# Kernel tuning notes

Hardware: AMD Instinct MI355X
Metric: run time of the kernel (lower is better)

Reference implementation:

```python
import jax, jax.numpy as jnp
import numpy as np

N = 8192          # number of particles
CUTOFF = 0.5      # self.cutoff (final filter uses d_ij <= cutoff)


def setup_inputs() -> dict:
    key = jax.random.key(0)
    k1, _ = jax.random.split(key)
    positions = jax.random.normal(k1, (N, 3), dtype=jnp.float32)
    box_vectors = jnp.eye(3, dtype=jnp.float32)  # orthogonal box, lengths 1.0
    iu, ju = np.triu_indices(N, k=1)             # all unique pairs i < j (as in _init_pairs)
    i_pairs = jnp.asarray(iu, dtype=jnp.int32)
    j_pairs = jnp.asarray(ju, dtype=jnp.int32)
    return {"positions": positions, "box_vectors": box_vectors,
            "i_pairs": i_pairs, "j_pairs": j_pairs, "is_periodic": 1}


def reference(positions, box_vectors, i_pairs, j_pairs, is_periodic):
    # OrthogonalDisplacementFunction: r_ij = x_i - x_j, wrapped into the box
    r_ij = positions[i_pairs] - positions[j_pairs]          # [P, 3]
    if is_periodic:
        box_lengths = jnp.diagonal(box_vectors)             # [3] (orthogonal box)
        half = box_lengths * 0.5
        r_ij = jnp.remainder(r_ij + half, box_lengths) - half
    d_ij = jnp.linalg.norm(r_ij, axis=1, keepdims=True)     # [P, 1]
    # Cutoff filter. torch compacts with boolean indexing (data-dependent shape);
    # for a jit-compatible fixed-shape reference we return a validity mask and
    # zero the entries of filtered-out pairs (only_unique_pairs=True branch).
    mask = d_ij[:, 0] <= CUTOFF                              # [P]
    pair_indices = jnp.stack([i_pairs, j_pairs])             # [2, P]
    r_out = jnp.where(mask[:, None], r_ij, 0.0)
    d_out = jnp.where(mask[:, None], d_ij, 0.0)
    return pair_indices, d_out, r_out, mask
```

## Files before the change

### kernel.cpp

```cpp
#include <hip/hip_runtime.h>
#include <math.h>


__device__ __forceinline__ float bf2f(unsigned short h) {
    return __uint_as_float(((unsigned)h) << 16);
}

__device__ __forceinline__ float rem_np(float x, float L) {
    float fm = fmodf(x, L);
    if (fm != 0.0f && ((fm < 0.0f) != (L < 0.0f))) fm += L;
    return fm;
}

__device__ __forceinline__ float rem1_np(float x) {
    float fm = __fsub_rn(x, truncf(x));
    if (fm < 0.0f) fm = __fadd_rn(fm, 1.0f);
    return fm;
}

template <bool F32>
__device__ __forceinline__ void load_pos(const void* __restrict__ pos, int idx,
                                         float& x, float& y, float& z) {
    if (F32) {
        const float* q = (const float*)pos + 3 * idx;
        x = q[0]; y = q[1]; z = q[2];
    } else {
        const unsigned short* q = (const unsigned short*)pos + 3 * idx;
        x = bf2f(q[0]); y = bf2f(q[1]); z = bf2f(q[2]);
    }
}

template <bool F32>
__device__ __forceinline__ void body(const void* __restrict__ pos,
                                     float Lx, float Ly, float Lz,
                                     bool periodic, bool unit, int N, long long P,
                                     int i, int j, long long t,
                                     float* __restrict__ out) {
    const float hx = __fmul_rn(Lx, 0.5f);
    const float hy = __fmul_rn(Ly, 0.5f);
    const float hz = __fmul_rn(Lz, 0.5f);

    float fi[4], fj[4], fd[4], fm[4], fr[12];

    float xi, yi, zi;
    load_pos<F32>(pos, i, xi, yi, zi);

#pragma unroll
    for (int k = 0; k < 4; ++k) {
        float xj, yj, zj;
        load_pos<F32>(pos, j, xj, yj, zj);
        float rx = __fsub_rn(xi, xj);
        float ry = __fsub_rn(yi, yj);
        float rz = __fsub_rn(zi, zj);
        if (periodic) {
            float vx = __fadd_rn(rx, hx);
            float vy = __fadd_rn(ry, hy);
            float vz = __fadd_rn(rz, hz);
            if (unit) {
                rx = __fsub_rn(rem1_np(vx), hx);
                ry = __fsub_rn(rem1_np(vy), hy);
                rz = __fsub_rn(rem1_np(vz), hz);
            } else {
                rx = __fsub_rn(rem_np(vx, Lx), hx);
                ry = __fsub_rn(rem_np(vy, Ly), hy);
                rz = __fsub_rn(rem_np(vz, Lz), hz);
            }
        }
        float d2 = __fadd_rn(__fadd_rn(__fmul_rn(rx, rx), __fmul_rn(ry, ry)),
                             __fmul_rn(rz, rz));
        float d = sqrtf(d2);
        bool m = (d <= 0.5f);

        fi[k] = (float)i;
        fj[k] = (float)j;
        fd[k] = m ? d : 0.0f;
        fm[k] = m ? 1.0f : 0.0f;
        fr[3 * k + 0] = m ? rx : 0.0f;
        fr[3 * k + 1] = m ? ry : 0.0f;
        fr[3 * k + 2] = m ? rz : 0.0f;

        if (k < 3) {
            ++j;
            if (j >= N) {
                ++i;
                j = i + 1;
                load_pos<F32>(pos, i, xi, yi, zi);
            }
        }
    }

    ((float4*)(out))[t]          = make_float4(fi[0], fi[1], fi[2], fi[3]);
    ((float4*)(out + P))[t]      = make_float4(fj[0], fj[1], fj[2], fj[3]);
    ((float4*)(out + 2 * P))[t]  = make_float4(fd[0], fd[1], fd[2], fd[3]);
    float4* orr = (float4*)(out + 3 * P);
    orr[3 * t + 0] = make_float4(fr[0], fr[1], fr[2], fr[3]);
    orr[3 * t + 1] = make_float4(fr[4], fr[5], fr[6], fr[7]);
    orr[3 * t + 2] = make_float4(fr[8], fr[9], fr[10], fr[11]);
    ((float4*)(out + 6 * P))[t]  = make_float4(fm[0], fm[1], fm[2], fm[3]);
}

__global__ __launch_bounds__(256) void nsq_kernel(const void* __restrict__ pos,
                                                  const unsigned* __restrict__ box_raw,
                                                  const int* __restrict__ isper,
                                                  float* __restrict__ out,
                                                  int N, long long P) {
    long long t = (long long)blockIdx.x * blockDim.x + threadIdx.x;
    long long p0 = t << 2;
    if (p0 >= P) return;

    const bool f32 = (box_raw[0] == 0x3F800000u);

    float Lx, Ly, Lz;
    if (f32) {
        const float* b = (const float*)box_raw;
        Lx = b[0]; Ly = b[4]; Lz = b[8];
    } else {
        const unsigned short* b = (const unsigned short*)box_raw;
        Lx = bf2f(b[0]); Ly = bf2f(b[4]); Lz = bf2f(b[8]);
    }
    const bool periodic = (isper[0] != 0);
    const bool unit = (Lx == 1.0f) && (Ly == 1.0f) && (Lz == 1.0f);

    const double M = 2.0 * (double)N - 1.0;
    int i = (int)((M - sqrt(M * M - 8.0 * (double)p0)) * 0.5);
    if (i < 0) i = 0;
    if (i > N - 2) i = N - 2;
    auto off = [N](long long a) { return a * (2LL * N - 1 - a) / 2; };
    while (i < N - 2 && off(i + 1) <= p0) ++i;
    while (i > 0 && off(i) > p0) --i;
    int j = (int)((long long)i + 1 + (p0 - off(i)));

    if (f32)
        body<true>(pos, Lx, Ly, Lz, periodic, unit, N, P, i, j, t, out);
    else
        body<false>(pos, Lx, Ly, Lz, periodic, unit, N, P, i, j, t, out);
}

extern "C" void kernel_launch(void* const* d_in, const int* in_sizes, int n_in,
                              void* d_out, int out_size, void* d_ws, size_t ws_size,
                              hipStream_t stream) {
    const void* pos = d_in[0];
    const unsigned* box = (const unsigned*)d_in[1];
    const int* isper = (const int*)d_in[4];

    long long P = (long long)out_size / 7;
    int N = in_sizes[0] / 3;

    long long nthreads = (P + 3) >> 2;
    int blocks = (int)((nthreads + 255) / 256);
    nsq_kernel<<<blocks, 256, 0, stream>>>(pos, box, isper, (float*)d_out, N, P);
}
```

Baseline: 1.029 ms.

## Stage bf16 positions in LDS with persistent tiles and coalesced r stores

Adds a persistent-grid kernel for the bf16 case that copies all particle positions into shared memory once per block, then loops over tiles of pairs reading positions from LDS. The displacement output is transposed through a shared buffer so r_ij is written with fully coalesced float4 stores. A grid-stride fallback kernel handles f32 or unsupported shapes, and both kernels are always launched, each exiting early when it is not the one responsible. The cost is an extra kernel launch, a large shared-memory footprint that limits occupancy, and two block barriers per tile.

Result: no change. 1.041 ms (+1.1%).

```diff
diff --git a/kernel.cpp b/kernel.cpp
--- a/kernel.cpp
+++ b/kernel.cpp
@@ -2,8 +2,19 @@
 #include <math.h>
 
 
+#define TPB 256
+#define PPT 4
+#define TILE (TPB * PPT)
+#define NMAX 8192
+
 __device__ __forceinline__ float bf2f(unsigned short h) {
     return __uint_as_float(((unsigned)h) << 16);
+}
+
+__device__ __forceinline__ float rem1_np(float x) {
+    float fm = __fsub_rn(x, truncf(x));
+    if (fm < 0.0f) fm = __fadd_rn(fm, 1.0f);
+    return fm;
 }
 
 __device__ __forceinline__ float rem_np(float x, float L) {
@@ -12,103 +23,186 @@
     return fm;
 }
 
-__device__ __forceinline__ float rem1_np(float x) {
-    float fm = __fsub_rn(x, truncf(x));
-    if (fm < 0.0f) fm = __fadd_rn(fm, 1.0f);
-    return fm;
-}
-
-template <bool F32>
-__device__ __forceinline__ void load_pos(const void* __restrict__ pos, int idx,
-                                         float& x, float& y, float& z) {
-    if (F32) {
-        const float* q = (const float*)pos + 3 * idx;
-        x = q[0]; y = q[1]; z = q[2];
-    } else {
-        const unsigned short* q = (const unsigned short*)pos + 3 * idx;
-        x = bf2f(q[0]); y = bf2f(q[1]); z = bf2f(q[2]);
-    }
-}
-
-template <bool F32>
-__device__ __forceinline__ void body(const void* __restrict__ pos,
-                                     float Lx, float Ly, float Lz,
-                                     bool periodic, bool unit, int N, long long P,
-                                     int i, int j, long long t,
-                                     float* __restrict__ out) {
-    const float hx = __fmul_rn(Lx, 0.5f);
-    const float hy = __fmul_rn(Ly, 0.5f);
-    const float hz = __fmul_rn(Lz, 0.5f);
-
-    float fi[4], fj[4], fd[4], fm[4], fr[12];
-
-    float xi, yi, zi;
-    load_pos<F32>(pos, i, xi, yi, zi);
-
-#pragma unroll
-    for (int k = 0; k < 4; ++k) {
-        float xj, yj, zj;
-        load_pos<F32>(pos, j, xj, yj, zj);
-        float rx = __fsub_rn(xi, xj);
-        float ry = __fsub_rn(yi, yj);
-        float rz = __fsub_rn(zi, zj);
-        if (periodic) {
-            float vx = __fadd_rn(rx, hx);
-            float vy = __fadd_rn(ry, hy);
-            float vz = __fadd_rn(rz, hz);
-            if (unit) {
-                rx = __fsub_rn(rem1_np(vx), hx);
-                ry = __fsub_rn(rem1_np(vy), hy);
-                rz = __fsub_rn(rem1_np(vz), hz);
+__device__ __forceinline__ void inv_tri(long long p0, int N, int& i, int& j) {
+    const double M = 2.0 * (double)N - 1.0;
+    int ii = (int)((M - sqrt(M * M - 8.0 * (double)p0)) * 0.5);
+    if (ii < 0) ii = 0;
+    if (ii > N - 2) ii = N - 2;
+    auto off = [N](long long a) { return a * (2LL * N - 1 - a) / 2; };
+    while (ii < N - 2 && off(ii + 1) <= p0) ++ii;
+    while (ii > 0 && off(ii) > p0) --ii;
+    i = ii;
+    j = (int)((long long)ii + 1 + (p0 - off(ii)));
+}
+
+__device__ __forceinline__ void pair_math(float xi, float yi, float zi,
+                                          float xj, float yj, float zj,
+                                          float hx, float hy, float hz,
+                                          float Lx, float Ly, float Lz,
+                                          bool periodic, bool unit,
+                                          float& rx, float& ry, float& rz,
+                                          float& d, bool& m) {
+    rx = __fsub_rn(xi, xj);
+    ry = __fsub_rn(yi, yj);
+    rz = __fsub_rn(zi, zj);
+    if (periodic) {
+        float vx = __fadd_rn(rx, hx), vy = __fadd_rn(ry, hy), vz = __fadd_rn(rz, hz);
+        if (unit) {
+            rx = __fsub_rn(rem1_np(vx), hx);
+            ry = __fsub_rn(rem1_np(vy), hy);
+            rz = __fsub_rn(rem1_np(vz), hz);
+        } else {
+            rx = __fsub_rn(rem_np(vx, Lx), hx);
+            ry = __fsub_rn(rem_np(vy, Ly), hy);
+            rz = __fsub_rn(rem_np(vz, Lz), hz);
+        }
+    }
+    float d2 = __fadd_rn(__fadd_rn(__fmul_rn(rx, rx), __fmul_rn(ry, ry)),
+                         __fmul_rn(rz, rz));
+    d = sqrtf(d2);
+    m = (d <= 0.5f);
+}
+
+__global__ __launch_bounds__(TPB) void nsq_bf16_lds(
+        const unsigned short* __restrict__ pos,
+        const unsigned* __restrict__ box_raw,
+        const int* __restrict__ isper,
+        float* __restrict__ out,
+        int N, long long P, int n_tiles) {
+    if (box_raw[0] == 0x3F800000u) return;
+
+    __shared__ unsigned short s_pos[3 * NMAX];
+    __shared__ float s_r[TPB * 13];
+
+    {
+        const uint4* src = (const uint4*)pos;
+        uint4* dst = (uint4*)s_pos;
+        int n16 = (3 * N) / 8;
+        for (int idx = threadIdx.x; idx < n16; idx += TPB) dst[idx] = src[idx];
+    }
+
+    const unsigned short* b = (const unsigned short*)box_raw;
+    const float Lx = bf2f(b[0]), Ly = bf2f(b[4]), Lz = bf2f(b[8]);
+    const float hx = __fmul_rn(Lx, 0.5f), hy = __fmul_rn(Ly, 0.5f), hz = __fmul_rn(Lz, 0.5f);
+    const bool periodic = (isper[0] != 0);
+    const bool unit = (Lx == 1.0f) && (Ly == 1.0f) && (Lz == 1.0f);
+
+    __syncthreads();
+
+    float* out_i = out;
+    float* out_j = out + P;
+    float* out_d = out + 2 * P;
+    float* out_r = out + 3 * P;
+    float* out_m = out + 6 * P;
+
+    for (int tile = blockIdx.x; tile < n_tiles; tile += gridDim.x) {
+        const long long tp0 = (long long)tile * TILE;
+        const long long p0 = tp0 + (long long)threadIdx.x * PPT;
+        const int vpairs = (int)((P - tp0 < (long long)TILE) ? (P - tp0) : (long long)TILE);
+
+        float fi[PPT], fj[PPT], fd[PPT], fm[PPT], fr[3 * PPT];
+
+        int i = 0, j = 1;
+        if (p0 < P) inv_tri(p0, N, i, j);
+
+        float xi = bf2f(s_pos[3 * i + 0]);
+        float yi = bf2f(s_pos[3 * i + 1]);
+        float zi = bf2f(s_pos[3 * i + 2]);
+
+#pragma unroll
+        for (int k = 0; k < PPT; ++k) {
+            const bool valid = (p0 + k) < P;
+            int jj = j < N ? j : (N - 1);
+            float xj = bf2f(s_pos[3 * jj + 0]);
+            float yj = bf2f(s_pos[3 * jj + 1]);
+            float zj = bf2f(s_pos[3 * jj + 2]);
+            float rx, ry, rz, d; bool m;
+            pair_math(xi, yi, zi, xj, yj, zj, hx, hy, hz, Lx, Ly, Lz,
+                      periodic, unit, rx, ry, rz, d, m);
+            m = m && valid;
+            fi[k] = valid ? (float)i : 0.0f;
+            fj[k] = valid ? (float)jj : 0.0f;
+            fd[k] = m ? d : 0.0f;
+            fm[k] = m ? 1.0f : 0.0f;
+            fr[3 * k + 0] = m ? rx : 0.0f;
+            fr[3 * k + 1] = m ? ry : 0.0f;
+            fr[3 * k + 2] = m ? rz : 0.0f;
+            if (k < PPT - 1) {
+                ++j;
+                if (j >= N) {
+                    if (i < N - 2) {
+                        ++i;
+                        j = i + 1;
+                        xi = bf2f(s_pos[3 * i + 0]);
+                        yi = bf2f(s_pos[3 * i + 1]);
+                        zi = bf2f(s_pos[3 * i + 2]);
+                    } else {
+                        j = N - 1;
+                    }
+                }
+            }
+        }
+
+        const long long t4 = p0 >> 2;
+        if (p0 + PPT <= P) {
+            ((float4*)out_i)[t4] = make_float4(fi[0], fi[1], fi[2], fi[3]);
+            ((float4*)out_j)[t4] = make_float4(fj[0], fj[1], fj[2], fj[3]);
+            ((float4*)out_d)[t4] = make_float4(fd[0], fd[1], fd[2], fd[3]);
+            ((float4*)out_m)[t4] = make_float4(fm[0], fm[1], fm[2], fm[3]);
+        } else if (p0 < P) {
+            for (int k = 0; k < PPT; ++k) {
+                if (p0 + k < P) {
+                    out_i[p0 + k] = fi[k];
+                    out_j[p0 + k] = fj[k];
+                    out_d[p0 + k] = fd[k];
+                    out_m[p0 + k] = fm[k];
+                }
+            }
+        }
+
+        __syncthreads();
+#pragma unroll
+        for (int k = 0; k < PPT; ++k) {
+            s_r[13 * threadIdx.x + 3 * k + 0] = fr[3 * k + 0];
+            s_r[13 * threadIdx.x + 3 * k + 1] = fr[3 * k + 1];
+            s_r[13 * threadIdx.x + 3 * k + 2] = fr[3 * k + 2];
+        }
+        __syncthreads();
+
+        const long long R0 = 3 * tp0;
+        const int vfloats = 3 * vpairs;
+#pragma unroll
+        for (int s = 0; s < 3; ++s) {
+            const int u0 = 4 * (s * TPB + threadIdx.x);
+            if (u0 + 3 < vfloats || (vpairs == TILE)) {
+                float v[4];
+#pragma unroll
+                for (int e = 0; e < 4; ++e) {
+                    int u = u0 + e, q = u / 3, c = u - 3 * q;
+                    v[e] = s_r[13 * (q >> 2) + 3 * (q & 3) + c];
+                }
+                ((float4*)(out_r + R0))[u0 >> 2] = make_float4(v[0], v[1], v[2], v[3]);
             } else {
-                rx = __fsub_rn(rem_np(vx, Lx), hx);
-                ry = __fsub_rn(rem_np(vy, Ly), hy);
-                rz = __fsub_rn(rem_np(vz, Lz), hz);
-            }
-        }
-        float d2 = __fadd_rn(__fadd_rn(__fmul_rn(rx, rx), __fmul_rn(ry, ry)),
-                             __fmul_rn(rz, rz));
-        float d = sqrtf(d2);
-        bool m = (d <= 0.5f);
-
-        fi[k] = (float)i;
-        fj[k] = (float)j;
-        fd[k] = m ? d : 0.0f;
-        fm[k] = m ? 1.0f : 0.0f;
-        fr[3 * k + 0] = m ? rx : 0.0f;
-        fr[3 * k + 1] = m ? ry : 0.0f;
-        fr[3 * k + 2] = m ? rz : 0.0f;
-
-        if (k < 3) {
-            ++j;
-            if (j >= N) {
-                ++i;
-                j = i + 1;
-                load_pos<F32>(pos, i, xi, yi, zi);
-            }
-        }
-    }
-
-    ((float4*)(out))[t]          = make_float4(fi[0], fi[1], fi[2], fi[3]);
-    ((float4*)(out + P))[t]      = make_float4(fj[0], fj[1], fj[2], fj[3]);
-    ((float4*)(out + 2 * P))[t]  = make_float4(fd[0], fd[1], fd[2], fd[3]);
-    float4* orr = (float4*)(out + 3 * P);
-    orr[3 * t + 0] = make_float4(fr[0], fr[1], fr[2], fr[3]);
-    orr[3 * t + 1] = make_float4(fr[4], fr[5], fr[6], fr[7]);
-    orr[3 * t + 2] = make_float4(fr[8], fr[9], fr[10], fr[11]);
-    ((float4*)(out + 6 * P))[t]  = make_float4(fm[0], fm[1], fm[2], fm[3]);
-}
-
-__global__ __launch_bounds__(256) void nsq_kernel(const void* __restrict__ pos,
-                                                  const unsigned* __restrict__ box_raw,
-                                                  const int* __restrict__ isper,
-                                                  float* __restrict__ out,
-                                                  int N, long long P) {
-    long long t = (long long)blockIdx.x * blockDim.x + threadIdx.x;
-    long long p0 = t << 2;
-    if (p0 >= P) return;
-
+                for (int e = 0; e < 4; ++e) {
+                    int u = u0 + e;
+                    if (u < vfloats) {
+                        int q = u / 3, c = u - 3 * q;
+                        out_r[R0 + u] = s_r[13 * (q >> 2) + 3 * (q & 3) + c];
+                    }
+                }
+            }
+        }
+    }
+}
+
+__global__ __launch_bounds__(TPB) void nsq_fallback(
+        const void* __restrict__ pos,
+        const unsigned* __restrict__ box_raw,
+        const int* __restrict__ isper,
+        float* __restrict__ out,
+        int N, long long P, int fast_handled) {
     const bool f32 = (box_raw[0] == 0x3F800000u);
+    if (fast_handled && !f32) return;
 
     float Lx, Ly, Lz;
     if (f32) {
@@ -118,22 +212,86 @@
         const unsigned short* b = (const unsigned short*)box_raw;
         Lx = bf2f(b[0]); Ly = bf2f(b[4]); Lz = bf2f(b[8]);
     }
+    const float hx = __fmul_rn(Lx, 0.5f), hy = __fmul_rn(Ly, 0.5f), hz = __fmul_rn(Lz, 0.5f);
     const bool periodic = (isper[0] != 0);
     const bool unit = (Lx == 1.0f) && (Ly == 1.0f) && (Lz == 1.0f);
 
-    const double M = 2.0 * (double)N - 1.0;
-    int i = (int)((M - sqrt(M * M - 8.0 * (double)p0)) * 0.5);
-    if (i < 0) i = 0;
-    if (i > N - 2) i = N - 2;
-    auto off = [N](long long a) { return a * (2LL * N - 1 - a) / 2; };
-    while (i < N - 2 && off(i + 1) <= p0) ++i;
-    while (i > 0 && off(i) > p0) --i;
-    int j = (int)((long long)i + 1 + (p0 - off(i)));
-
-    if (f32)
-        body<true>(pos, Lx, Ly, Lz, periodic, unit, N, P, i, j, t, out);
-    else
-        body<false>(pos, Lx, Ly, Lz, periodic, unit, N, P, i, j, t, out);
+    const float* pf = (const float*)pos;
+    const unsigned short* ph = (const unsigned short*)pos;
+
+    float* out_i = out;
+    float* out_j = out + P;
+    float* out_d = out + 2 * P;
+    float* out_r = out + 3 * P;
+    float* out_m = out + 6 * P;
+
+    const long long tmax = (P + PPT - 1) / PPT;
+    const long long stride = (long long)gridDim.x * blockDim.x;
+    for (long long t = (long long)blockIdx.x * blockDim.x + threadIdx.x;
+         t < tmax; t += stride) {
+        const long long p0 = t * PPT;
+        int i, j;
+        inv_tri(p0, N, i, j);
+
+        float fi[PPT], fj[PPT], fd[PPT], fm[PPT], fr[3 * PPT];
+
+        float xi, yi, zi;
+        if (f32) { xi = pf[3 * i]; yi = pf[3 * i + 1]; zi = pf[3 * i + 2]; }
+        else     { xi = bf2f(ph[3 * i]); yi = bf2f(ph[3 * i + 1]); zi = bf2f(ph[3 * i + 2]); }
+
+#pragma unroll
+        for (int k = 0; k < PPT; ++k) {
+            const bool valid = (p0 + k) < P;
+            int jj = j < N ? j : (N - 1);
+            float xj, yj, zj;
+            if (f32) { xj = pf[3 * jj]; yj = pf[3 * jj + 1]; zj = pf[3 * jj + 2]; }
+            else     { xj = bf2f(ph[3 * jj]); yj = bf2f(ph[3 * jj + 1]); zj = bf2f(ph[3 * jj + 2]); }
+            float rx, ry, rz, d; bool m;
+            pair_math(xi, yi, zi, xj, yj, zj, hx, hy, hz, Lx, Ly, Lz,
+                      periodic, unit, rx, ry, rz, d, m);
+            m = m && valid;
+            fi[k] = valid ? (float)i : 0.0f;
+            fj[k] = valid ? (float)jj : 0.0f;
+            fd[k] = m ? d : 0.0f;
+            fm[k] = m ? 1.0f : 0.0f;
+            fr[3 * k + 0] = m ? rx : 0.0f;
+            fr[3 * k + 1] = m ? ry : 0.0f;
+            fr[3 * k + 2] = m ? rz : 0.0f;
+            if (k < PPT - 1) {
+                ++j;
+                if (j >= N) {
+                    if (i < N - 2) {
+                        ++i; j = i + 1;
+                        if (f32) { xi = pf[3 * i]; yi = pf[3 * i + 1]; zi = pf[3 * i + 2]; }
+                        else     { xi = bf2f(ph[3 * i]); yi = bf2f(ph[3 * i + 1]); zi = bf2f(ph[3 * i + 2]); }
+                    } else j = N - 1;
+                }
+            }
+        }
+
+        if (p0 + PPT <= P) {
+            ((float4*)out_i)[t] = make_float4(fi[0], fi[1], fi[2], fi[3]);
+            ((float4*)out_j)[t] = make_float4(fj[0], fj[1], fj[2], fj[3]);
+            ((float4*)out_d)[t] = make_float4(fd[0], fd[1], fd[2], fd[3]);
+            ((float4*)out_m)[t] = make_float4(fm[0], fm[1], fm[2], fm[3]);
+            float4* orr = (float4*)(out_r);
+            orr[3 * t + 0] = make_float4(fr[0], fr[1], fr[2], fr[3]);
+            orr[3 * t + 1] = make_float4(fr[4], fr[5], fr[6], fr[7]);
+            orr[3 * t + 2] = make_float4(fr[8], fr[9], fr[10], fr[11]);
+        } else {
+            for (int k = 0; k < PPT; ++k) {
+                if (p0 + k < P) {
+                    out_i[p0 + k] = fi[k];
+                    out_j[p0 + k] = fj[k];
+                    out_d[p0 + k] = fd[k];
+                    out_m[p0 + k] = fm[k];
+                    out_r[3 * (p0 + k) + 0] = fr[3 * k + 0];
+                    out_r[3 * (p0 + k) + 1] = fr[3 * k + 1];
+                    out_r[3 * (p0 + k) + 2] = fr[3 * k + 2];
+                }
+            }
+        }
+    }
 }
 
 extern "C" void kernel_launch(void* const* d_in, const int* in_sizes, int n_in,
@@ -143,10 +301,17 @@
     const unsigned* box = (const unsigned*)d_in[1];
     const int* isper = (const int*)d_in[4];
 
-    long long P = (long long)out_size / 7;
-    int N = in_sizes[0] / 3;
-
-    long long nthreads = (P + 3) >> 2;
-    int blocks = (int)((nthreads + 255) / 256);
-    nsq_kernel<<<blocks, 256, 0, stream>>>(pos, box, isper, (float*)d_out, N, P);
-}
+    const long long P = (long long)out_size / 7;
+    const int N = in_sizes[0] / 3;
+
+    const int fast_ok = (N <= NMAX) && (N % 8 == 0) && (P % 4 == 0);
+    const int n_tiles = (int)((P + TILE - 1) / TILE);
+
+    if (fast_ok) {
+        int blocks = n_tiles < 512 ? n_tiles : 512;
+        nsq_bf16_lds<<<blocks, TPB, 0, stream>>>(
+            (const unsigned short*)pos, box, isper, (float*)d_out, N, P, n_tiles);
+    }
+    nsq_fallback<<<1024, TPB, 0, stream>>>(pos, box, isper, (float*)d_out,
+                                           N, P, fast_ok);
+}
```
